# Kernel tuning notes

Measured on AMD Instinct MI355X. Metric: run time of the kernel, lower is better.

The kernel has to match this reference:

```python
import jax, jax.numpy as jnp
import numpy as np

B, N, M, D = 2, 256, 8, 256      # batch, seq, modalities, dmodel
H, DH = 8, 64                     # heads, dim_head (hardcoded defaults)
INNER = H * DH                    # 512
MULT = 4                          # FFN mult
SCALE = DH ** -0.5
EPS = 1e-5


def layer_norm(x, g, b):
    mu = jnp.mean(x, axis=-1, keepdims=True)
    var = jnp.mean((x - mu) ** 2, axis=-1, keepdims=True)
    return (x - mu) * jax.lax.rsqrt(var + EPS) * g + b


def setup_inputs() -> dict:
    key = jax.random.key(0)
    ks = jax.random.split(key, 8)
    s = 0.02
    return {
        "x": jax.random.normal(ks[0], (B, D, M, N), jnp.float32),
        "Wq": jax.random.normal(ks[1], (D, INNER), jnp.float32) * s,
        "Wkv": jax.random.normal(ks[2], (D, 2 * INNER), jnp.float32) * s,
        "Wout": jax.random.normal(ks[3], (INNER * M, D * M), jnp.float32) * s,
        "bout": jnp.zeros((D * M,), jnp.float32),
        "g1": jnp.ones((D,), jnp.float32),
        "beta1": jnp.zeros((D,), jnp.float32),
        "Wff1": jax.random.normal(ks[4], (D, 2 * D * MULT), jnp.float32) * s,
        "bff1": jnp.zeros((2 * D * MULT,), jnp.float32),
        "Wff2": jax.random.normal(ks[5], (D * MULT, D), jnp.float32) * s,
        "bff2": jnp.zeros((D,), jnp.float32),
        "g2": jnp.ones((D,), jnp.float32),
        "beta2": jnp.zeros((D,), jnp.float32),
    }


def reference(x, Wq, Wkv, Wout, bout, g1, beta1, Wff1, bff1, Wff2, bff2, g2, beta2):
    x_shape = x.shape
    xt = jnp.transpose(x, (0, 3, 2, 1))          # [B,N,M,D]
    # --- Channel_Seq_Big_Attention (self-attention, context = x) ---
    q = (xt @ Wq).reshape(B, N, M, H, DH)
    kv = xt @ Wkv
    k, v = jnp.split(kv, 2, axis=-1)
    k = k.reshape(B, N, M, H, DH)
    v = v.reshape(B, N, M, H, DH)
    # sim: [(b h), i, j, m, z] kept as [B,H,i,j,m,z]
    sim = jnp.einsum('bimhd,bjzhd->bhijmz', q, k) * SCALE
    attn = jax.nn.softmax(sim, axis=2)           # softmax over j (dim=-3 of bijmz)
    out = jnp.einsum('bhijmz,bjmhd->bizhd', attn, v)  # [B,N,M,H,DH]
    out = out.reshape(B, N, M * H * DH)          # 'b n (m h d)'
    o = (out @ Wout + bout).reshape(B, N, M, D)
    # --- residual + post-norm ---
    xt = layer_norm(xt + o, g1, beta1)
    # --- GEGLU FFN ---
    hg = xt @ Wff1 + bff1
    a, gate = jnp.split(hg, 2, axis=-1)
    ff = (a * jax.nn.gelu(gate, approximate=False)) @ Wff2 + bff2
    xt = layer_norm(xt + ff, g2, beta2)
    return xt.reshape(x_shape)                   # torch .view(x_shape)
```

## Files before the change

### kernel.cpp

```cpp
#include <hip/hip_runtime.h>
#include <math.h>

#define KS_ 0.1803368801111244f

typedef __attribute__((ext_vector_type(8))) short bf16x8;
typedef __attribute__((ext_vector_type(4))) short bf16x4;
typedef __attribute__((ext_vector_type(4))) float f32x4;

__device__ inline short f2bf(float f) {
  unsigned u = __builtin_bit_cast(unsigned, f);
  u += 0x7fff + ((u >> 16) & 1);
  return (short)(u >> 16);
}

__device__ inline void wt_tile(const float* __restrict__ W, short* __restrict__ WT,
                               int K, int N, int bx, int by, int t, float (*tile)[33]) {
  int n0 = bx * 32, k0 = by * 32;
  int tx = t & 31, ty = t >> 5;
#pragma unroll
  for (int r = 0; r < 32; r += 8)
    tile[ty + r][tx] = W[(size_t)(k0 + ty + r) * N + n0 + tx];
  __syncthreads();
#pragma unroll
  for (int r = 0; r < 32; r += 8)
    WT[(size_t)(n0 + ty + r) * K + k0 + tx] = f2bf(tile[tx][ty + r]);
}

__global__ __launch_bounds__(256) void k_prep_all(const float* __restrict__ x, float* __restrict__ xt,
                                                  short* __restrict__ xtbf,
                                                  const float* __restrict__ Wq, const float* __restrict__ Wkv,
                                                  const float* __restrict__ Wout, const float* __restrict__ Wff1,
                                                  const float* __restrict__ Wff2,
                                                  short* __restrict__ WqkvT, short* __restrict__ WoutT,
                                                  short* __restrict__ Wff1T, short* __restrict__ Wff2T) {
  __shared__ float tile[32][33];
  int bid = blockIdx.x, t = threadIdx.x;
  if (bid < 8192) {
    wt_tile(Wout, WoutT, 4096, 2048, bid & 63, bid >> 6, t, tile);
  } else if (bid < 9216) {
    int r = bid - 8192;
    int bx = r & 7, by = (r >> 3) & 7, bm = r >> 6;
    int b = bm >> 3, m = bm & 7;
    int d0 = bx * 32, n0 = by * 32;
    int tx = t & 31, ty = t >> 5;
#pragma unroll
    for (int rr = 0; rr < 32; rr += 8) {
      int d = d0 + ty + rr, n = n0 + tx;
      tile[ty + rr][tx] = x[((size_t)(b * 256 + d) * 8 + m) * 256 + n];
    }
    __syncthreads();
#pragma unroll
    for (int rr = 0; rr < 32; rr += 8) {
      int n = n0 + ty + rr, d = d0 + tx;
      float v = tile[tx][ty + rr];
      size_t idx = ((size_t)(b * 256 + n) * 8 + m) * 256 + d;
      xt[idx] = v;
      xtbf[idx] = f2bf(v);
    }
  } else if (bid < 9344) {
    int r = bid - 9216;
    wt_tile(Wq, WqkvT, 256, 512, r & 15, r >> 4, t, tile);
  } else if (bid < 9600) {
    int r = bid - 9344;
    wt_tile(Wkv, WqkvT + 131072, 256, 1024, r & 31, r >> 5, t, tile);
  } else if (bid < 10112) {
    int r = bid - 9600;
    wt_tile(Wff1, Wff1T, 256, 2048, r & 63, r >> 6, t, tile);
  } else {
    int r = bid - 10112;
    wt_tile(Wff2, Wff2T, 1024, 256, r & 7, r >> 3, t, tile);
  }
}

__global__ __launch_bounds__(256) void k_gemm_bf(const short* __restrict__ A, const short* __restrict__ Bt,
                                                 const float* __restrict__ bias, float* __restrict__ C,
                                                 int M, int N, int K, int Ks) {
  __shared__ short As[64 * 40];
  __shared__ short Bs[64 * 40];
  int t = threadIdx.x;
  int row0 = blockIdx.y * 64, col0 = blockIdx.x * 64;
  int kp = blockIdx.z;
  int kbeg = kp * Ks, kend = kbeg + Ks;
  int w = t >> 6, lane = t & 63, quad = lane >> 4, l16 = lane & 15;
  int wr = w >> 1, wc = w & 1;
  int lrow = t >> 2, lch = (t & 3) * 8;
  const short* Ap = A + (size_t)(row0 + lrow) * K + lch;
  const short* Bp = Bt + (size_t)(col0 + lrow) * K + lch;
  f32x4 acc[2][2] = {{{0,0,0,0},{0,0,0,0}},{{0,0,0,0},{0,0,0,0}}};
  bf16x8 av = *(const bf16x8*)(Ap + kbeg);
  bf16x8 bv = *(const bf16x8*)(Bp + kbeg);
  for (int k0 = kbeg; k0 < kend; k0 += 32) {
    *(bf16x8*)&As[lrow * 40 + lch] = av;
    *(bf16x8*)&Bs[lrow * 40 + lch] = bv;
    __syncthreads();
    if (k0 + 32 < kend) {
      av = *(const bf16x8*)(Ap + k0 + 32);
      bv = *(const bf16x8*)(Bp + k0 + 32);
    }
    bf16x8 af[2], bf[2];
#pragma unroll
    for (int rf = 0; rf < 2; rf++) af[rf] = *(const bf16x8*)&As[(wr * 32 + rf * 16 + l16) * 40 + quad * 8];
#pragma unroll
    for (int cf = 0; cf < 2; cf++) bf[cf] = *(const bf16x8*)&Bs[(wc * 32 + cf * 16 + l16) * 40 + quad * 8];
#pragma unroll
    for (int rf = 0; rf < 2; rf++)
#pragma unroll
      for (int cf = 0; cf < 2; cf++)
        acc[rf][cf] = __builtin_amdgcn_mfma_f32_16x16x32_bf16(af[rf], bf[cf], acc[rf][cf], 0, 0, 0);
    __syncthreads();
  }
  float* Cp = C + (size_t)kp * M * N;
#pragma unroll
  for (int rf = 0; rf < 2; rf++)
#pragma unroll
    for (int cf = 0; cf < 2; cf++) {
      int col = col0 + wc * 32 + cf * 16 + l16;
      float vb = (bias && kp == 0) ? bias[col] : 0.0f;
#pragma unroll
      for (int r = 0; r < 4; r++) {
        int row = row0 + wr * 32 + rf * 16 + quad * 4 + r;
        Cp[(size_t)row * N + col] = acc[rf][cf][r] + vb;
      }
    }
}

__global__ __launch_bounds__(256) void k_ff1g(const short* __restrict__ A, const short* __restrict__ Bt,
                                              const float* __restrict__ bias, short* __restrict__ gg) {
  __shared__ short As[64 * 40];
  __shared__ short Ba[64 * 40];
  __shared__ short Bg[64 * 40];
  int t = threadIdx.x;
  int colA0 = blockIdx.x * 64, row0 = blockIdx.y * 64;
  int w = t >> 6, lane = t & 63, quad = lane >> 4, l16 = lane & 15;
  int wr = w >> 1, wc = w & 1;
  int lrow = t >> 2, lch = (t & 3) * 8;
  const short* Ap  = A + (size_t)(row0 + lrow) * 256 + lch;
  const short* Bpa = Bt + (size_t)(colA0 + lrow) * 256 + lch;
  const short* Bpg = Bt + (size_t)(1024 + colA0 + lrow) * 256 + lch;
  f32x4 za = {0, 0, 0, 0};
  f32x4 acc_a[2][2] = {{za, za}, {za, za}};
  f32x4 acc_g[2][2] = {{za, za}, {za, za}};
  bf16x8 av = *(const bf16x8*)(Ap);
  bf16x8 bva = *(const bf16x8*)(Bpa);
  bf16x8 bvg = *(const bf16x8*)(Bpg);
  for (int k0 = 0; k0 < 256; k0 += 32) {
    *(bf16x8*)&As[lrow * 40 + lch] = av;
    *(bf16x8*)&Ba[lrow * 40 + lch] = bva;
    *(bf16x8*)&Bg[lrow * 40 + lch] = bvg;
    __syncthreads();
    if (k0 + 32 < 256) {
      av  = *(const bf16x8*)(Ap + k0 + 32);
      bva = *(const bf16x8*)(Bpa + k0 + 32);
      bvg = *(const bf16x8*)(Bpg + k0 + 32);
    }
    bf16x8 af[2], ba[2], bg[2];
#pragma unroll
    for (int rf = 0; rf < 2; rf++) af[rf] = *(const bf16x8*)&As[(wr * 32 + rf * 16 + l16) * 40 + quad * 8];
#pragma unroll
    for (int cf = 0; cf < 2; cf++) {
      ba[cf] = *(const bf16x8*)&Ba[(wc * 32 + cf * 16 + l16) * 40 + quad * 8];
      bg[cf] = *(const bf16x8*)&Bg[(wc * 32 + cf * 16 + l16) * 40 + quad * 8];
    }
#pragma unroll
    for (int rf = 0; rf < 2; rf++)
#pragma unroll
      for (int cf = 0; cf < 2; cf++) {
        acc_a[rf][cf] = __builtin_amdgcn_mfma_f32_16x16x32_bf16(af[rf], ba[cf], acc_a[rf][cf], 0, 0, 0);
        acc_g[rf][cf] = __builtin_amdgcn_mfma_f32_16x16x32_bf16(af[rf], bg[cf], acc_g[rf][cf], 0, 0, 0);
      }
    __syncthreads();
  }
#pragma unroll
  for (int rf = 0; rf < 2; rf++)
#pragma unroll
    for (int cf = 0; cf < 2; cf++) {
      int col = colA0 + wc * 32 + cf * 16 + l16;
      float ba_ = bias[col], bg_ = bias[1024 + col];
#pragma unroll
      for (int r = 0; r < 4; r++) {
        int row = row0 + wr * 32 + rf * 16 + quad * 4 + r;
        float a = acc_a[rf][cf][r] + ba_;
        float g = acc_g[rf][cf][r] + bg_;
        float ge = 0.5f * g * (1.0f + erff(g * 0.70710678118654752f));
        gg[(size_t)row * 1024 + col] = f2bf(a * ge);
      }
    }
}

__global__ __launch_bounds__(256) void k_prep_qk(const float* __restrict__ qkv, short* __restrict__ qfrag,
                                                 short* __restrict__ kfrag) {
  int bid = blockIdx.x;
  int sel = bid >> 10;
  int c = (bid & 1023) * 256 + threadIdx.x;
  int lane = c & 63, ks = (c >> 6) & 1, rt = (c >> 7) & 127, bh = c >> 14;
  int b = bh >> 3, h = bh & 7;
  int mz = rt >> 4, ij = ((rt & 15) << 4) + (lane & 15);
  int d = ks * 32 + (lane >> 4) * 8;
  const float* src = qkv + (size_t)((b * 256 + ij) * 8 + mz) * 1536 + sel * 512 + h * 64 + d;
  float4 f0 = *(const float4*)src, f1 = *(const float4*)(src + 4);
  bf16x8 o;
  o[0] = f2bf(f0.x); o[1] = f2bf(f0.y); o[2] = f2bf(f0.z); o[3] = f2bf(f0.w);
  o[4] = f2bf(f1.x); o[5] = f2bf(f1.y); o[6] = f2bf(f1.z); o[7] = f2bf(f1.w);
  short* dst = sel ? kfrag : qfrag;
  *(bf16x8*)(dst + (size_t)c * 8) = o;
}

__global__ __launch_bounds__(256) void k_prep_vfrag(const float* __restrict__ qkv, short* __restrict__ vfrag) {
  __shared__ float Vs[256 * 66];
  int jc = blockIdx.x, bh = blockIdx.y;
  int b = bh >> 3, h = bh & 7;
  int t = threadIdx.x;
#pragma unroll
  for (int cc = 0; cc < 16; cc++) {
    int c = cc * 256 + t;
    int row = c >> 4, ch = c & 15;
    int m = row >> 5, jl = row & 31;
    float4 f = *(const float4*)(qkv + (size_t)((b * 256 + jc * 32 + jl) * 8 + m) * 1536 + 1024 + h * 64 + ch * 4);
    *(float4*)&Vs[row * 66 + ch * 4] = f;
  }
  __syncthreads();
  int m0 = t >> 6, lane = t & 63, quad = lane >> 4, l16 = lane & 15;
#pragma unroll
  for (int dt = 0; dt < 4; dt++)
#pragma unroll
    for (int jf = 0; jf < 2; jf++) {
      bf16x8 o;
#pragma unroll
      for (int e = 0; e < 8; e++) {
        int row = (2 * m0 + (e >> 2)) * 32 + jf * 16 + quad * 4 + (e & 3);
        o[e] = f2bf(Vs[row * 66 + dt * 16 + l16]);
      }
      size_t cid = ((((size_t)(bh * 8 + jc) * 4 + m0) * 4 + dt) * 2 + jf) * 64 + lane;
      *(bf16x8*)(vfrag + cid * 8) = o;
    }
}

__global__ __launch_bounds__(256) void k_attn_den5(const short* __restrict__ qfrag, const short* __restrict__ kfrag,
                                                   float* __restrict__ rdg) {
  int ct2 = blockIdx.x, mp = blockIdx.y, bh = blockIdx.z;
  int t = threadIdx.x;
  int w = t >> 6, lane = t & 63;
  int rt0 = ct2 * 8 + w * 2;
  bf16x8 bfr[2][2];
#pragma unroll
  for (int cf = 0; cf < 2; cf++)
#pragma unroll
    for (int ks = 0; ks < 2; ks++)
      bfr[cf][ks] = *(const bf16x8*)(kfrag + ((size_t)((bh * 128 + rt0 + cf) * 2 + ks)) * 512 + lane * 8);
  for (int mi = 0; mi < 2; mi++) {
    int m = mp * 2 + mi;
    float fa0 = 0.0f, fa1 = 0.0f;
#pragma unroll 4
    for (int it2 = 0; it2 < 16; it2++) {
      const short* ap = qfrag + ((size_t)((bh * 128 + m * 16 + it2) * 2)) * 512 + lane * 8;
      bf16x8 a0 = *(const bf16x8*)ap;
      bf16x8 a1 = *(const bf16x8*)(ap + 512);
      f32x4 c0 = {0, 0, 0, 0}, c1 = {0, 0, 0, 0};
      c0 = __builtin_amdgcn_mfma_f32_16x16x32_bf16(a0, bfr[0][0], c0, 0, 0, 0);
      c0 = __builtin_amdgcn_mfma_f32_16x16x32_bf16(a1, bfr[0][1], c0, 0, 0, 0);
      c1 = __builtin_amdgcn_mfma_f32_16x16x32_bf16(a0, bfr[1][0], c1, 0, 0, 0);
      c1 = __builtin_amdgcn_mfma_f32_16x16x32_bf16(a1, bfr[1][1], c1, 0, 0, 0);
#pragma unroll
      for (int r = 0; r < 4; r++) {
        fa0 += __builtin_amdgcn_exp2f(c0[r] * KS_);
        fa1 += __builtin_amdgcn_exp2f(c1[r] * KS_);
      }
    }
    fa0 += __shfl_xor(fa0, 16); fa0 += __shfl_xor(fa0, 32);
    fa1 += __shfl_xor(fa1, 16); fa1 += __shfl_xor(fa1, 32);
    if (lane < 16) {
      rdg[(size_t)(bh * 8 + m) * 2048 + rt0 * 16 + lane] = -__builtin_amdgcn_logf(fa0);
      rdg[(size_t)(bh * 8 + m) * 2048 + (rt0 + 1) * 16 + lane] = -__builtin_amdgcn_logf(fa1);
    }
  }
}

__global__ __launch_bounds__(256) void k_attn_out6(const short* __restrict__ qfrag, const short* __restrict__ kfrag,
                                                   const short* __restrict__ vfrag, const float* __restrict__ rdg,
                                                   short* __restrict__ ao) {
  __shared__ float red[4 * 64 * 17];
  int z = blockIdx.x, itp = blockIdx.y, bh = blockIdx.z;
  int b = bh >> 3, h = bh & 7;
  int t = threadIdx.x, w = t >> 6, lane = t & 63, quad = lane >> 4, l16 = lane & 15;
  const float* rb = rdg + (size_t)bh * 16384;
  f32x4 z4 = {0, 0, 0, 0};
  bf16x8 qf[2][2][2];
#pragma unroll
  for (int iti = 0; iti < 2; iti++)
#pragma unroll
    for (int mm = 0; mm < 2; mm++)
#pragma unroll
      for (int ks = 0; ks < 2; ks++)
        qf[iti][mm][ks] = *(const bf16x8*)(qfrag +
            ((size_t)((bh * 128 + (2 * w + mm) * 16 + itp * 2 + iti) * 2 + ks)) * 512 + lane * 8);
  f32x4 acc[2][4];
#pragma unroll
  for (int iti = 0; iti < 2; iti++)
#pragma unroll
    for (int dt = 0; dt < 4; dt++) acc[iti][dt] = z4;
  bf16x8 vf[4][2], kf[2][2];
  float4 nv0[2], nv1[2];
#pragma unroll
  for (int dt = 0; dt < 4; dt++)
#pragma unroll
    for (int jf = 0; jf < 2; jf++)
      vf[dt][jf] = *(const bf16x8*)(vfrag + ((((size_t)(bh * 8 + 0) * 4 + w) * 4 + dt) * 2 + jf) * 512 + lane * 8);
#pragma unroll
  for (int jf = 0; jf < 2; jf++) {
    const short* kp = kfrag + ((size_t)((bh * 128 + z * 16 + 0 * 2 + jf) * 2)) * 512 + lane * 8;
    kf[jf][0] = *(const bf16x8*)kp;
    kf[jf][1] = *(const bf16x8*)(kp + 512);
    nv0[jf] = *(const float4*)(rb + (size_t)(2 * w) * 2048 + z * 256 + 0 * 32 + jf * 16 + quad * 4);
    nv1[jf] = *(const float4*)(rb + (size_t)(2 * w + 1) * 2048 + z * 256 + 0 * 32 + jf * 16 + quad * 4);
  }
  for (int jc = 0; jc < 8; jc++) {
    bf16x8 vfn[4][2], kfn[2][2];
    float4 nv0n[2], nv1n[2];
    if (jc < 7) {
      int jn = jc + 1;
#pragma unroll
      for (int dt = 0; dt < 4; dt++)
#pragma unroll
        for (int jf = 0; jf < 2; jf++)
          vfn[dt][jf] = *(const bf16x8*)(vfrag + ((((size_t)(bh * 8 + jn) * 4 + w) * 4 + dt) * 2 + jf) * 512 + lane * 8);
#pragma unroll
      for (int jf = 0; jf < 2; jf++) {
        const short* kp = kfrag + ((size_t)((bh * 128 + z * 16 + jn * 2 + jf) * 2)) * 512 + lane * 8;
        kfn[jf][0] = *(const bf16x8*)kp;
        kfn[jf][1] = *(const bf16x8*)(kp + 512);
        nv0n[jf] = *(const float4*)(rb + (size_t)(2 * w) * 2048 + z * 256 + jn * 32 + jf * 16 + quad * 4);
        nv1n[jf] = *(const float4*)(rb + (size_t)(2 * w + 1) * 2048 + z * 256 + jn * 32 + jf * 16 + quad * 4);
      }
    }
    float n0[2][4] = {{nv0[0].x, nv0[0].y, nv0[0].z, nv0[0].w}, {nv0[1].x, nv0[1].y, nv0[1].z, nv0[1].w}};
    float n1[2][4] = {{nv1[0].x, nv1[0].y, nv1[0].z, nv1[0].w}, {nv1[1].x, nv1[1].y, nv1[1].z, nv1[1].w}};
#pragma unroll
    for (int iti = 0; iti < 2; iti++) {
      f32x4 c[2][2] = {{z4, z4}, {z4, z4}};
#pragma unroll
      for (int jf = 0; jf < 2; jf++)
#pragma unroll
        for (int mm = 0; mm < 2; mm++) {
          c[jf][mm] = __builtin_amdgcn_mfma_f32_16x16x32_bf16(kf[jf][0], qf[iti][mm][0], c[jf][mm], 0, 0, 0);
          c[jf][mm] = __builtin_amdgcn_mfma_f32_16x16x32_bf16(kf[jf][1], qf[iti][mm][1], c[jf][mm], 0, 0, 0);
        }
      bf16x8 pf[2];
#pragma unroll
      for (int jf = 0; jf < 2; jf++) {
        unsigned u[8];
#pragma unroll
        for (int e = 0; e < 4; e++) {
          u[e]     = __builtin_bit_cast(unsigned, __builtin_amdgcn_exp2f(fmaf(c[jf][0][e], KS_, n0[jf][e]))) + 0x8000u;
          u[e + 4] = __builtin_bit_cast(unsigned, __builtin_amdgcn_exp2f(fmaf(c[jf][1][e], KS_, n1[jf][e]))) + 0x8000u;
        }
        uint4 pv;
        pv.x = __builtin_amdgcn_perm(u[1], u[0], 0x07060302u);
        pv.y = __builtin_amdgcn_perm(u[3], u[2], 0x07060302u);
        pv.z = __builtin_amdgcn_perm(u[5], u[4], 0x07060302u);
        pv.w = __builtin_amdgcn_perm(u[7], u[6], 0x07060302u);
        pf[jf] = __builtin_bit_cast(bf16x8, pv);
      }
#pragma unroll
      for (int dt = 0; dt < 4; dt++)
#pragma unroll
        for (int jf = 0; jf < 2; jf++)
          acc[iti][dt] = __builtin_amdgcn_mfma_f32_16x16x32_bf16(vf[dt][jf], pf[jf], acc[iti][dt], 0, 0, 0);
    }
    if (jc < 7) {
#pragma unroll
      for (int dt = 0; dt < 4; dt++)
#pragma unroll
        for (int jf = 0; jf < 2; jf++) vf[dt][jf] = vfn[dt][jf];
#pragma unroll
      for (int jf = 0; jf < 2; jf++) {
        kf[jf][0] = kfn[jf][0]; kf[jf][1] = kfn[jf][1];
        nv0[jf] = nv0n[jf]; nv1[jf] = nv1n[jf];
      }
    }
  }
  for (int iti = 0; iti < 2; iti++) {
#pragma unroll
    for (int dt = 0; dt < 4; dt++)
#pragma unroll
      for (int r = 0; r < 4; r++)
        red[w * 1088 + (dt * 16 + quad * 4 + r) * 17 + l16] = acc[iti][dt][r];
    __syncthreads();
    {
      int i = t >> 4, dg = t & 15;
      float s[4] = {0, 0, 0, 0};
#pragma unroll
      for (int w2 = 0; w2 < 4; w2++)
#pragma unroll
        for (int r2 = 0; r2 < 4; r2++)
          s[r2] += red[w2 * 1088 + (dg * 4 + r2) * 17 + i];
      bf16x4 ov;
#pragma unroll
      for (int r2 = 0; r2 < 4; r2++) ov[r2] = f2bf(s[r2]);
      *(bf16x4*)(ao + (size_t)((b * 256 + itp * 32 + iti * 16 + i) * 8 + z) * 512 + h * 64 + dg * 4) = ov;
    }
    __syncthreads();
  }
}

__global__ __launch_bounds__(256) void k_ln(const float* __restrict__ X, const float* __restrict__ P, int np,
                                            const float* __restrict__ g, const float* __restrict__ be,
                                            float* __restrict__ Y, short* __restrict__ Ybf) {
  __shared__ float sm[8];
  int row = blockIdx.x, t = threadIdx.x;
  int lane = t & 63, w = t >> 6;
  size_t base = (size_t)row * 256;
  float v = X[base + t];
  for (int p = 0; p < np; p++) v += P[(size_t)p * 1048576 + base + t];
  float s = v;
  s += __shfl_xor(s, 1); s += __shfl_xor(s, 2); s += __shfl_xor(s, 4);
  s += __shfl_xor(s, 8); s += __shfl_xor(s, 16); s += __shfl_xor(s, 32);
  if (lane == 0) sm[w] = s;
  __syncthreads();
  float mu = (sm[0] + sm[1] + sm[2] + sm[3]) * (1.0f / 256.0f);
  float dv = v - mu;
  float s2 = dv * dv;
  s2 += __shfl_xor(s2, 1); s2 += __shfl_xor(s2, 2); s2 += __shfl_xor(s2, 4);
  s2 += __shfl_xor(s2, 8); s2 += __shfl_xor(s2, 16); s2 += __shfl_xor(s2, 32);
  if (lane == 0) sm[4 + w] = s2;
  __syncthreads();
  float var = (sm[4] + sm[5] + sm[6] + sm[7]) * (1.0f / 256.0f);
  float rs = rsqrtf(var + 1e-5f);
  float res = dv * rs * g[t] + be[t];
  Y[base + t] = res;
  if (Ybf) Ybf[base + t] = f2bf(res);
}

extern "C" void kernel_launch(void* const* d_in, const int* in_sizes, int n_in,
                              void* d_out, int out_size, void* d_ws, size_t ws_size,
                              hipStream_t stream) {
  const float* x    = (const float*)d_in[0];
  const float* Wq   = (const float*)d_in[1];
  const float* Wkv  = (const float*)d_in[2];
  const float* Wout = (const float*)d_in[3];
  const float* bout = (const float*)d_in[4];
  const float* g1   = (const float*)d_in[5];
  const float* be1  = (const float*)d_in[6];
  const float* Wff1 = (const float*)d_in[7];
  const float* bff1 = (const float*)d_in[8];
  const float* Wff2 = (const float*)d_in[9];
  const float* bff2 = (const float*)d_in[10];
  const float* g2   = (const float*)d_in[11];
  const float* be2  = (const float*)d_in[12];
  float* out = (float*)d_out;
  float* w = (float*)d_ws;

  float* xt   = w;
  float* qkv  = w + 1048576;
  float* part = w + 1048576;
  float* y    = w + 9437184;
  float* rdg  = w + 11534336;
  short* sb     = (short*)(w + 11796480);
  short* qfrag  = sb;
  short* kfrag  = sb + 2097152;
  short* vfrag  = sb + 4194304;
  short* xt_bf  = sb + 6291456;
  short* ao_bf  = sb + 7340032;
  short* y_bf   = sb + 9437184;
  short* gg_bf  = sb + 10485760;
  short* WqkvT  = sb + 14680064;
  short* WoutT  = sb + 15073280;
  short* Wff1T  = sb + 23461888;
  short* Wff2T  = sb + 23986176;

  k_prep_all<<<10368, 256, 0, stream>>>(x, xt, xt_bf, Wq, Wkv, Wout, Wff1, Wff2,
                                        WqkvT, WoutT, Wff1T, Wff2T);
  k_gemm_bf<<<dim3(24, 64, 1), 256, 0, stream>>>(xt_bf, WqkvT, nullptr, qkv, 4096, 1536, 256, 256);
  k_prep_qk<<<2048, 256, 0, stream>>>(qkv, qfrag, kfrag);
  k_prep_vfrag<<<dim3(8, 16), 256, 0, stream>>>(qkv, vfrag);
  k_attn_den5<<<dim3(16, 4, 16), 256, 0, stream>>>(qfrag, kfrag, rdg);
  k_attn_out6<<<dim3(8, 8, 16), 256, 0, stream>>>(qfrag, kfrag, vfrag, rdg, ao_bf);
  k_gemm_bf<<<dim3(32, 8, 4), 256, 0, stream>>>(ao_bf, WoutT, bout, part, 512, 2048, 4096, 1024);
  k_ln<<<4096, 256, 0, stream>>>(xt, part, 4, g1, be1, y, y_bf);
  k_ff1g<<<dim3(16, 64), 256, 0, stream>>>(y_bf, Wff1T, bff1, gg_bf);
  k_gemm_bf<<<dim3(4, 64, 4), 256, 0, stream>>>(gg_bf, Wff2T, bff2, part, 4096, 256, 1024, 256);
  k_ln<<<4096, 256, 0, stream>>>(y, part, 4, g2, be2, out, nullptr);
}
```

Before: 230.9 us.

## Fuse QKV projection GEMM with bf16 fragment packing for attention

```diff
diff --git a/kernel.cpp b/kernel.cpp
--- a/kernel.cpp
+++ b/kernel.cpp
@@ -69,6 +69,103 @@
   } else {
     int r = bid - 10112;
     wt_tile(Wff2, Wff2T, 1024, 256, r & 7, r >> 3, t, tile);
+  }
+}
+
+__global__ __launch_bounds__(256) void k_gemm_qkv(const short* __restrict__ A, const short* __restrict__ Bt,
+                                                  short* __restrict__ qfrag, short* __restrict__ kfrag,
+                                                  short* __restrict__ vfrag) {
+  __shared__ short As[64 * 40];
+  __shared__ short Bs[64 * 40];
+  __shared__ short Cs[64 * 72];
+  int t = threadIdx.x;
+  int bx = blockIdx.x, by = blockIdx.y;
+  int sel = bx >> 3, h = bx & 7;
+  int row0 = by * 64, col0 = bx * 64;
+  int b = by >> 5, n0 = (by * 8) & 255;
+  int bh = b * 8 + h;
+  int w = t >> 6, lane = t & 63, quad = lane >> 4, l16 = lane & 15;
+  int wr = w >> 1, wc = w & 1;
+  int lrow = t >> 2, lch = (t & 3) * 8;
+  const short* Ap = A + (size_t)(row0 + lrow) * 256 + lch;
+  const short* Bp = Bt + (size_t)(col0 + lrow) * 256 + lch;
+  f32x4 acc[2][2] = {{{0,0,0,0},{0,0,0,0}},{{0,0,0,0},{0,0,0,0}}};
+  bf16x8 av = *(const bf16x8*)(Ap);
+  bf16x8 bv = *(const bf16x8*)(Bp);
+  for (int k0 = 0; k0 < 256; k0 += 32) {
+    *(bf16x8*)&As[lrow * 40 + lch] = av;
+    *(bf16x8*)&Bs[lrow * 40 + lch] = bv;
+    __syncthreads();
+    if (k0 + 32 < 256) {
+      av = *(const bf16x8*)(Ap + k0 + 32);
+      bv = *(const bf16x8*)(Bp + k0 + 32);
+    }
+    bf16x8 af[2], bf[2];
+#pragma unroll
+    for (int rf = 0; rf < 2; rf++) af[rf] = *(const bf16x8*)&As[(wr * 32 + rf * 16 + l16) * 40 + quad * 8];
+#pragma unroll
+    for (int cf = 0; cf < 2; cf++) bf[cf] = *(const bf16x8*)&Bs[(wc * 32 + cf * 16 + l16) * 40 + quad * 8];
+#pragma unroll
+    for (int rf = 0; rf < 2; rf++)
+#pragma unroll
+      for (int cf = 0; cf < 2; cf++)
+        acc[rf][cf] = __builtin_amdgcn_mfma_f32_16x16x32_bf16(af[rf], bf[cf], acc[rf][cf], 0, 0, 0);
+    __syncthreads();
+  }
+  if (sel < 2) {
+#pragma unroll
+    for (int rf = 0; rf < 2; rf++)
+#pragma unroll
+      for (int cf = 0; cf < 2; cf++) {
+        int col = wc * 32 + cf * 16 + l16;
+#pragma unroll
+        for (int r = 0; r < 4; r++)
+          Cs[(wr * 32 + rf * 16 + quad * 4 + r) * 72 + col] = f2bf(acc[rf][cf][r]);
+      }
+  } else {
+#pragma unroll
+    for (int rf = 0; rf < 2; rf++)
+#pragma unroll
+      for (int cf = 0; cf < 2; cf++) {
+        int col = wc * 32 + cf * 16 + l16;
+        bf16x4 pk;
+#pragma unroll
+        for (int r = 0; r < 4; r++) pk[r] = f2bf(acc[rf][cf][r]);
+        *(bf16x4*)&Cs[col * 72 + wr * 32 + rf * 16 + quad * 4] = pk;
+      }
+  }
+  __syncthreads();
+  if (sel < 2) {
+    short* dst = sel ? kfrag : qfrag;
+    int it = n0 >> 4, l16b = n0 & 8;
+#pragma unroll
+    for (int cidx = 0; cidx < 2; cidx++) {
+      int chunk = t + cidx * 256;
+      int m = chunk >> 6, ks2 = (chunk >> 5) & 1, q2 = (chunk >> 3) & 3, n = chunk & 7;
+      bf16x8 val = *(const bf16x8*)&Cs[(n * 8 + m) * 72 + ks2 * 32 + q2 * 8];
+      size_t off = ((size_t)(bh * 128 + m * 16 + it) * 2 + ks2) * 512 + (q2 * 16 + l16b + n) * 8;
+      *(bf16x8*)(dst + off) = val;
+    }
+  } else {
+    int jc = n0 >> 5, jf = (n0 >> 4) & 1, qbase = (n0 & 8) >> 2;
+#pragma unroll
+    for (int cidx = 0; cidx < 2; cidx++) {
+      int chunk = t + cidx * 256;
+      int qd = chunk >> 8, m0 = (chunk >> 6) & 3, dtt = (chunk >> 4) & 3, l16c = chunk & 15;
+      int d = dtt * 16 + l16c;
+      unsigned u[4];
+#pragma unroll
+      for (int e3 = 0; e3 < 4; e3++)
+        u[e3] = *(const unsigned*)&Cs[d * 72 + qd * 32 + e3 * 8 + 2 * m0];
+      uint4 pv;
+      pv.x = __builtin_amdgcn_perm(u[1], u[0], 0x05040100u);
+      pv.y = __builtin_amdgcn_perm(u[3], u[2], 0x05040100u);
+      pv.z = __builtin_amdgcn_perm(u[1], u[0], 0x07060302u);
+      pv.w = __builtin_amdgcn_perm(u[3], u[2], 0x07060302u);
+      int quad2 = qbase + qd;
+      size_t cid = (((size_t)(bh * 8 + jc) * 4 + m0) * 4 + dtt) * 2 + jf;
+      *(bf16x8*)(vfrag + cid * 512 + (quad2 * 16 + l16c) * 8) = __builtin_bit_cast(bf16x8, pv);
+    }
   }
 }
 
@@ -184,54 +281,6 @@
         float ge = 0.5f * g * (1.0f + erff(g * 0.70710678118654752f));
         gg[(size_t)row * 1024 + col] = f2bf(a * ge);
       }
-    }
-}
-
-__global__ __launch_bounds__(256) void k_prep_qk(const float* __restrict__ qkv, short* __restrict__ qfrag,
-                                                 short* __restrict__ kfrag) {
-  int bid = blockIdx.x;
-  int sel = bid >> 10;
-  int c = (bid & 1023) * 256 + threadIdx.x;
-  int lane = c & 63, ks = (c >> 6) & 1, rt = (c >> 7) & 127, bh = c >> 14;
-  int b = bh >> 3, h = bh & 7;
-  int mz = rt >> 4, ij = ((rt & 15) << 4) + (lane & 15);
-  int d = ks * 32 + (lane >> 4) * 8;
-  const float* src = qkv + (size_t)((b * 256 + ij) * 8 + mz) * 1536 + sel * 512 + h * 64 + d;
-  float4 f0 = *(const float4*)src, f1 = *(const float4*)(src + 4);
-  bf16x8 o;
-  o[0] = f2bf(f0.x); o[1] = f2bf(f0.y); o[2] = f2bf(f0.z); o[3] = f2bf(f0.w);
-  o[4] = f2bf(f1.x); o[5] = f2bf(f1.y); o[6] = f2bf(f1.z); o[7] = f2bf(f1.w);
-  short* dst = sel ? kfrag : qfrag;
-  *(bf16x8*)(dst + (size_t)c * 8) = o;
-}
-
-__global__ __launch_bounds__(256) void k_prep_vfrag(const float* __restrict__ qkv, short* __restrict__ vfrag) {
-  __shared__ float Vs[256 * 66];
-  int jc = blockIdx.x, bh = blockIdx.y;
-  int b = bh >> 3, h = bh & 7;
-  int t = threadIdx.x;
-#pragma unroll
-  for (int cc = 0; cc < 16; cc++) {
-    int c = cc * 256 + t;
-    int row = c >> 4, ch = c & 15;
-    int m = row >> 5, jl = row & 31;
-    float4 f = *(const float4*)(qkv + (size_t)((b * 256 + jc * 32 + jl) * 8 + m) * 1536 + 1024 + h * 64 + ch * 4);
-    *(float4*)&Vs[row * 66 + ch * 4] = f;
-  }
-  __syncthreads();
-  int m0 = t >> 6, lane = t & 63, quad = lane >> 4, l16 = lane & 15;
-#pragma unroll
-  for (int dt = 0; dt < 4; dt++)
-#pragma unroll
-    for (int jf = 0; jf < 2; jf++) {
-      bf16x8 o;
-#pragma unroll
-      for (int e = 0; e < 8; e++) {
-        int row = (2 * m0 + (e >> 2)) * 32 + jf * 16 + quad * 4 + (e & 3);
-        o[e] = f2bf(Vs[row * 66 + dt * 16 + l16]);
-      }
-      size_t cid = ((((size_t)(bh * 8 + jc) * 4 + m0) * 4 + dt) * 2 + jf) * 64 + lane;
-      *(bf16x8*)(vfrag + cid * 8) = o;
     }
 }
 
@@ -450,7 +499,6 @@
   float* w = (float*)d_ws;
 
   float* xt   = w;
-  float* qkv  = w + 1048576;
   float* part = w + 1048576;
   float* y    = w + 9437184;
   float* rdg  = w + 11534336;
@@ -469,9 +517,7 @@
 
   k_prep_all<<<10368, 256, 0, stream>>>(x, xt, xt_bf, Wq, Wkv, Wout, Wff1, Wff2,
                                         WqkvT, WoutT, Wff1T, Wff2T);
-  k_gemm_bf<<<dim3(24, 64, 1), 256, 0, stream>>>(xt_bf, WqkvT, nullptr, qkv, 4096, 1536, 256, 256);
-  k_prep_qk<<<2048, 256, 0, stream>>>(qkv, qfrag, kfrag);
-  k_prep_vfrag<<<dim3(8, 16), 256, 0, stream>>>(qkv, vfrag);
+  k_gemm_qkv<<<dim3(24, 64), 256, 0, stream>>>(xt_bf, WqkvT, qfrag, kfrag, vfrag);
   k_attn_den5<<<dim3(16, 4, 16), 256, 0, stream>>>(qfrag, kfrag, rdg);
   k_attn_out6<<<dim3(8, 8, 16), 256, 0, stream>>>(qfrag, kfrag, vfrag, rdg, ao_bf);
   k_gemm_bf<<<dim3(32, 8, 4), 256, 0, stream>>>(ao_bf, WoutT, bout, part, 512, 2048, 4096, 1024);
```

Measured after the change: 217.9 us. 1.06x faster.
